# Kernel tuning notes

Hardware: AMD Instinct MI355X
Metric: run time of the kernel (lower is better)

## Reference

```python
import jax, jax.numpy as jnp
import numpy as np

N_WAY = 5
N_SHOT = 25
N_SUPPORT = N_WAY * N_SHOT  # 125
N_QUERY = 2048
D = 8192
C_REG = 0.1        # default C_reg of MetaOptNetHead_SVM_CS
MAX_ITER = 20      # default maxIter of QPFunction
SIGMA = 0.1        # centering parameter of the interior-point iteration


def setup_inputs() -> dict:
    key = jax.random.key(0)
    k1, k2, k3 = jax.random.split(key, 3)
    query = jax.random.normal(k1, (N_QUERY, D), dtype=jnp.float32)
    support = jax.random.normal(k2, (N_SUPPORT, D), dtype=jnp.float32)
    support_labels = jax.random.randint(k3, (N_SUPPORT,), 0, N_WAY, dtype=jnp.int32)
    scale = jnp.ones((1,), dtype=jnp.float32)  # nn.Parameter([1.0])
    return {
        "query": query,
        "support": support,
        "support_labels": support_labels,
        "n_way": N_WAY,
        "n_shot": N_SHOT,
        "scale": scale,
    }


def _solve_qp(G, e, h, A, b):
    """Solve min_z 0.5 z^T G z + e^T z  s.t.  z <= h (C = I),  A z = b.

    Primal-dual infeasible-start interior-point method with MAX_ITER fixed
    Newton steps (the jax analogue of qpth's QPFunction(maxIter=20)).
    Shapes: G (B,n,n), e (B,n), h (B,n), A (B,p,n), b (B,p).
    """
    B, n = e.shape
    p = b.shape[1]
    m = n  # C = I -> one inequality per variable
    At = jnp.swapaxes(A, 1, 2)                      # (B,n,p)
    zero_pp = jnp.zeros((B, p, p), dtype=G.dtype)
    A_row = jnp.concatenate([A, zero_pp], axis=2)   # (B,p,n+p), constant

    z = jnp.zeros_like(e)
    s = jnp.ones_like(h)
    lam = jnp.ones_like(h)
    nu = jnp.zeros_like(b)

    def frac_to_boundary(x, dx):
        # largest alpha in (0,1] keeping x + alpha*dx > 0
        ratio = jnp.where(dx < 0, -x / jnp.where(dx < 0, dx, -1.0), jnp.inf)
        return jnp.min(ratio, axis=1)

    def step(carry, _):
        z, s, lam, nu = carry
        Gz = jnp.einsum('bij,bj->bi', G, z)
        r1 = Gz + e + lam + jnp.einsum('bpi,bp->bi', A, nu)   # dual residual (C^T lam = lam)
        r2 = z + s - h                                         # primal ineq residual
        r4 = jnp.einsum('bpi,bi->bp', A, z) - b                # primal eq residual
        mu = SIGMA * jnp.sum(s * lam, axis=1, keepdims=True) / m
        r3 = lam * s - mu                                      # perturbed complementarity
        # Reduced KKT system: (G + diag(lam/s)) dz + A^T dnu = rhs1 ; A dz = -r4
        H = G + jax.vmap(jnp.diag)(lam / s)                    # (B,n,n)
        rhs1 = -(r1 + (lam * r2 - r3) / s)                     # (B,n)
        K = jnp.concatenate(
            [jnp.concatenate([H, At], axis=2), A_row], axis=1)  # (B,n+p,n+p)
        rhs = jnp.concatenate([rhs1, -r4], axis=1)             # (B,n+p)
        sol = jnp.linalg.solve(K, rhs[..., None])[..., 0]
        dz, dnu = sol[:, :n], sol[:, n:]
        ds = -r2 - dz
        dlam = (-r3 - lam * ds) / s
        alpha = jnp.minimum(
            1.0, 0.99 * jnp.minimum(frac_to_boundary(s, ds),
                                    frac_to_boundary(lam, dlam)))[:, None]
        return (z + alpha * dz, s + alpha * ds,
                lam + alpha * dlam, nu + alpha * dnu), None

    (z, s, lam, nu), _ = jax.lax.scan(step, (z, s, lam, nu), None, length=MAX_ITER)
    return z


def _svm_cs_head(query, support, support_labels, n_way):
    support_b = support[None]            # (1, ns, d) -- head unsqueezes batch dim
    query_b = query[None]                # (1, nq, d)
    B, ns, _ = support_b.shape
    f32 = jnp.float32

    # Gram matrix of support, then kron with I_{n_way} (batched_kronecker == jnp.kron)
    K = jnp.einsum('bnd,bmd->bnm', support_b, support_b)            # (B,ns,ns)
    eye_w = jnp.eye(n_way, dtype=f32)
    G = jax.vmap(lambda k: jnp.kron(k, eye_w))(K)                    # (B,ns*nw,ns*nw)
    G = G + jnp.eye(n_way * ns, dtype=f32)[None]

    y1h = jax.nn.one_hot(support_labels, n_way, dtype=f32).reshape(B, ns * n_way)
    e = -y1h
    h = C_REG * y1h
    A = jnp.kron(jnp.eye(ns, dtype=f32), jnp.ones((1, n_way), f32))[None]  # (1,ns,ns*nw)
    b = jnp.zeros((B, ns), f32)

    qp_sol = _solve_qp(G, e, h, A, b)                                # (B, ns*nw)

    compat = jnp.einsum('bnd,bqd->bnq', support_b, query_b)          # (B,ns,nq)
    qp3 = qp_sol.reshape(B, ns, n_way)
    # logits[b,q,w] = sum_s qp3[b,s,w] * compat[b,s,q]
    logits = jnp.einsum('bsw,bsq->bqw', qp3, compat)                 # (B,nq,nw)
    num_sv = jnp.sum(jnp.any(qp3 > 0.001, axis=2))                   # support-vector count
    return logits, num_sv


def reference(query, support, support_labels, n_way, n_shot, scale):
    logits, num_sv = _svm_cs_head(query, support, support_labels, n_way)
    return scale * logits, num_sv
```

## Files before the change

kernel.cpp:

```cpp
#include <hip/hip_runtime.h>

#define NS   125
#define NW   5
#define NQ   2048
#define DD   8192
#define CREG 0.1f
#define PGD_ITERS 16

#define OFF_PART 0
#define OFF_K    1000000
#define OFF_QP3  1016000
#define OFF_W    1017000

__global__ __launch_bounds__(256) void gram_partial(const float* __restrict__ support,
                                                    float* __restrict__ part) {
    __shared__ __align__(16) float As[128][68];
    __shared__ __align__(16) float Bs[128][68];
    const int tid = threadIdx.x;
    const int c  = blockIdx.x;
    const int qy = blockIdx.y, qz = blockIdx.z;
    const int d0 = c * 128;
    const int sy0 = qy * 64, sz0 = qz * 64;
    for (int idx = tid; idx < 64 * 128; idx += 256) {
        int sl = idx >> 7, dj = idx & 127;
        int sa = sy0 + sl, sb = sz0 + sl;
        As[dj][sl] = (sa < NS) ? support[(size_t)sa * DD + d0 + dj] : 0.f;
        Bs[dj][sl] = (sb < NS) ? support[(size_t)sb * DD + d0 + dj] : 0.f;
    }
    __syncthreads();
    const int tx = tid & 15, ty = tid >> 4;
    float acc[4][4];
#pragma unroll
    for (int i = 0; i < 4; i++)
#pragma unroll
        for (int j = 0; j < 4; j++) acc[i][j] = 0.f;
#pragma unroll 4
    for (int d = 0; d < 128; ++d) {
        float4 a = *(const float4*)&As[d][tx * 4];
        float4 b = *(const float4*)&Bs[d][ty * 4];
        float av[4] = {a.x, a.y, a.z, a.w};
        float bv[4] = {b.x, b.y, b.z, b.w};
#pragma unroll
        for (int i = 0; i < 4; i++)
#pragma unroll
            for (int j = 0; j < 4; j++) acc[i][j] += av[i] * bv[j];
    }
    float* dst = part + (size_t)c * (NS * NS);
#pragma unroll
    for (int i = 0; i < 4; i++) {
        int gi = sy0 + tx * 4 + i;
        if (gi >= NS) continue;
#pragma unroll
        for (int j = 0; j < 4; j++) {
            int gj = sz0 + ty * 4 + j;
            if (gj < NS) dst[gi * NS + gj] = acc[i][j];
        }
    }
}

__global__ __launch_bounds__(256) void gram_reduce(const float* __restrict__ part,
                                                   float* __restrict__ Kg) {
    int t = blockIdx.x * 256 + threadIdx.x;
    if (t < NS * NS) {
        float s = 0.f;
        for (int c = 0; c < 64; ++c) s += part[(size_t)c * (NS * NS) + t];
        Kg[t] = s;
    }
}

__global__ __launch_bounds__(256) void qp_solve(const float* __restrict__ Kg,
                                                const int* __restrict__ labels,
                                                float* __restrict__ qp3,
                                                float* __restrict__ outNumSv) {
    __shared__ __align__(16) float zs[NW][128];
    __shared__ float red2[128 * 25];
    __shared__ float rsmax[2];
    __shared__ int svcount;

    const int tid  = threadIdx.x;
    const int w    = tid >> 6;
    const int lane = tid & 63;
    const int c0   = w * 32;
    const int r0   = lane, r1 = lane + 64;

    float kr0[32], kr1[32];
#pragma unroll
    for (int j = 0; j < 32; ++j) {
        const int col = c0 + j;
        const bool cv = (col < NS);
        kr0[j] = cv ? Kg[col * NS + r0] : 0.f;
        kr1[j] = (cv && r1 < NS) ? Kg[col * NS + r1] : 0.f;
    }
    for (int idx = tid; idx < NW * 128; idx += 256) ((float*)zs)[idx] = 0.f;
    if (tid == 0) svcount = 0;
    float rsum0 = 0.f, rsum1 = 0.f;
#pragma unroll
    for (int j = 0; j < 32; ++j) { rsum0 += fabsf(kr0[j]); rsum1 += fabsf(kr1[j]); }
    red2[r0 * 25 + w * 5] = rsum0;
    red2[r1 * 25 + w * 5] = rsum1;
    __syncthreads();
    const int prow = w * 64 + lane;
    if (w < 2) {
        const float* rr = &red2[prow * 25];
        float t = (prow < NS) ? rr[0] + rr[5] + rr[10] + rr[15] : 0.f;
#pragma unroll
        for (int off = 32; off; off >>= 1) t = fmaxf(t, __shfl_xor(t, off));
        if (lane == 0) rsmax[w] = t;
    }
    __syncthreads();
    const float eta = 1.9f / (fmaxf(rsmax[0], rsmax[1]) + 1.0f);
    const int lab = (w < 2 && prow < NS) ? labels[prow] : 0;
    float z[NW] = {0.f, 0.f, 0.f, 0.f, 0.f};

    for (int it = 0; it < PGD_ITERS; ++it) {
        float acc0[NW] = {0.f, 0.f, 0.f, 0.f, 0.f};
        float acc1[NW] = {0.f, 0.f, 0.f, 0.f, 0.f};
#pragma unroll
        for (int c = 0; c < 8; ++c) {
            const int jb = c0 + 4 * c;
            float4 z0 = *(const float4*)&zs[0][jb];
            float4 z1 = *(const float4*)&zs[1][jb];
            float4 z2 = *(const float4*)&zs[2][jb];
            float4 z3 = *(const float4*)&zs[3][jb];
            float4 z4 = *(const float4*)&zs[4][jb];
            const float k00 = kr0[4*c], k01 = kr0[4*c+1], k02 = kr0[4*c+2], k03 = kr0[4*c+3];
            const float k10 = kr1[4*c], k11 = kr1[4*c+1], k12 = kr1[4*c+2], k13 = kr1[4*c+3];
            acc0[0] += k00*z0.x + k01*z0.y + k02*z0.z + k03*z0.w;
            acc0[1] += k00*z1.x + k01*z1.y + k02*z1.z + k03*z1.w;
            acc0[2] += k00*z2.x + k01*z2.y + k02*z2.z + k03*z2.w;
            acc0[3] += k00*z3.x + k01*z3.y + k02*z3.z + k03*z3.w;
            acc0[4] += k00*z4.x + k01*z4.y + k02*z4.z + k03*z4.w;
            acc1[0] += k10*z0.x + k11*z0.y + k12*z0.z + k13*z0.w;
            acc1[1] += k10*z1.x + k11*z1.y + k12*z1.z + k13*z1.w;
            acc1[2] += k10*z2.x + k11*z2.y + k12*z2.z + k13*z2.w;
            acc1[3] += k10*z3.x + k11*z3.y + k12*z3.z + k13*z3.w;
            acc1[4] += k10*z4.x + k11*z4.y + k12*z4.z + k13*z4.w;
        }
        {
            float* b0 = &red2[r0 * 25 + w * 5];
            b0[0] = acc0[0]; b0[1] = acc0[1]; b0[2] = acc0[2]; b0[3] = acc0[3]; b0[4] = acc0[4];
            float* b1 = &red2[r1 * 25 + w * 5];
            b1[0] = acc1[0]; b1[1] = acc1[1]; b1[2] = acc1[2]; b1[3] = acc1[3]; b1[4] = acc1[4];
        }
        __syncthreads();
        if (w < 2 && prow < NS) {
            const float* rr = &red2[prow * 25];
            float v[NW], h[NW];
#pragma unroll
            for (int a = 0; a < NW; a++) {
                float kz = rr[a] + rr[5 + a] + rr[10 + a] + rr[15 + a];
                float g = kz + z[a] - ((a == lab) ? 1.f : 0.f);
                v[a] = z[a] - eta * g;
                h[a] = (a == lab) ? CREG : 0.f;
            }
            float tau = fmaxf(fmaxf(fmaxf(v[0], v[1]), fmaxf(v[2], v[3])), v[4]);
#pragma unroll
            for (int n = 0; n < 7; ++n) {
                float g = 0.f, nf = 0.f;
#pragma unroll
                for (int a = 0; a < NW; a++) {
                    float d = v[a] - tau;
                    bool fr = (d <= h[a]);
                    g += fr ? d : h[a];
                    nf += fr ? 1.f : 0.f;
                }
                tau += g / nf;
            }
#pragma unroll
            for (int a = 0; a < NW; a++) {
                z[a] = fminf(v[a] - tau, h[a]);
                zs[a][prow] = z[a];
            }
        }
        __syncthreads();
    }

    if (w < 2 && prow < NS) {
        float m = fmaxf(fmaxf(fmaxf(z[0], z[1]), fmaxf(z[2], z[3])), z[4]);
        if (m > 0.001f) atomicAdd(&svcount, 1);
#pragma unroll
        for (int a = 0; a < NW; a++) qp3[prow * NW + a] = z[a];
    }
    __syncthreads();
    if (tid == 0) *outNumSv = (float)svcount;
}

__global__ __launch_bounds__(128) void w_kernel(const float* __restrict__ support,
                                                const float* __restrict__ qp3,
                                                float* __restrict__ W) {
    __shared__ float q3[NS * NW];
    const int tid = threadIdx.x;
    for (int i = tid; i < NS * NW; i += 128) q3[i] = qp3[i];
    __syncthreads();
    const int d = blockIdx.x * 128 + tid;
    float acc[NW] = {0.f, 0.f, 0.f, 0.f, 0.f};
    for (int sld = 0; sld < NS; ++sld) {
        float sv = support[(size_t)sld * DD + d];
#pragma unroll
        for (int a = 0; a < NW; a++) acc[a] += sv * q3[sld * NW + a];
    }
#pragma unroll
    for (int a = 0; a < NW; a++) W[(size_t)a * DD + d] = acc[a];
}

__global__ __launch_bounds__(256) void logits_kernel(const float* __restrict__ query,
                                                     const float* __restrict__ W,
                                                     const float* __restrict__ scale,
                                                     float* __restrict__ out) {
    const int tid = threadIdx.x;
    const int wave = tid >> 6, lane = tid & 63;
    const int q0 = blockIdx.x * 16 + wave * 4;
    float acc[4][NW];
#pragma unroll
    for (int j = 0; j < 4; j++)
#pragma unroll
        for (int a = 0; a < NW; a++) acc[j][a] = 0.f;
    const float4* qp[4];
#pragma unroll
    for (int j = 0; j < 4; j++) qp[j] = (const float4*)(query + (size_t)(q0 + j) * DD);
    for (int it = 0; it < 32; ++it) {
        int dv = it * 64 + lane;
        float4 qv[4];
#pragma unroll
        for (int j = 0; j < 4; j++) qv[j] = qp[j][dv];
#pragma unroll
        for (int a = 0; a < NW; a++) {
            float4 wv = ((const float4*)(W + (size_t)a * DD))[dv];
#pragma unroll
            for (int j = 0; j < 4; j++)
                acc[j][a] += qv[j].x * wv.x + qv[j].y * wv.y + qv[j].z * wv.z + qv[j].w * wv.w;
        }
    }
#pragma unroll
    for (int off = 32; off; off >>= 1) {
#pragma unroll
        for (int j = 0; j < 4; j++)
#pragma unroll
            for (int a = 0; a < NW; a++) acc[j][a] += __shfl_xor(acc[j][a], off);
    }
    if (lane == 0) {
        float sc = scale[0];
#pragma unroll
        for (int j = 0; j < 4; j++)
#pragma unroll
            for (int a = 0; a < NW; a++) out[(q0 + j) * NW + a] = sc * acc[j][a];
    }
}

extern "C" void kernel_launch(void* const* d_in, const int* in_sizes, int n_in,
                              void* d_out, int out_size, void* d_ws, size_t ws_size,
                              hipStream_t stream) {
    const float* query   = (const float*)d_in[0];
    const float* support = (const float*)d_in[1];
    const int*   labels  = (const int*)d_in[2];
    const float* scale   = (const float*)d_in[5];
    float* out = (float*)d_out;
    float* ws  = (float*)d_ws;

    float* part = ws + OFF_PART;
    float* Kg   = ws + OFF_K;
    float* qp3  = ws + OFF_QP3;
    float* W    = ws + OFF_W;

    hipLaunchKernelGGL(gram_partial, dim3(64, 2, 2), dim3(256), 0, stream, support, part);
    hipLaunchKernelGGL(gram_reduce, dim3(62), dim3(256), 0, stream, part, Kg);
    hipLaunchKernelGGL(qp_solve, dim3(1), dim3(256), 0, stream, Kg, labels, qp3, out + NQ * NW);
    hipLaunchKernelGGL(w_kernel, dim3(DD / 128), dim3(128), 0, stream, support, qp3, W);
    hipLaunchKernelGGL(logits_kernel, dim3(NQ / 16), dim3(256), 0, stream, query, W, scale, out);
}
```

Measured before the change: 195.0 us.

## Split logits GEMV over D into four chunks with separate reduction kernel

The logits kernel now splits the 8192-long dot products into four D-chunks, each block handling 8 queries (2 per wave) instead of 16, giving 1024 blocks instead of 128. Partial sums go to workspace and a small finish kernel adds the four partials and applies the scale. The aim is to spread the 64MB query read across more CUs to reach higher memory bandwidth, at the cost of an extra launch, a small partial-buffer round trip, and more repeated reads of W.

```diff
diff --git a/kernel.cpp b/kernel.cpp
--- a/kernel.cpp
+++ b/kernel.cpp
@@ -11,6 +11,7 @@
 #define OFF_K    1000000
 #define OFF_QP3  1016000
 #define OFF_W    1017000
+#define OFF_LP   1060000
 
 __global__ __launch_bounds__(256) void gram_partial(const float* __restrict__ support,
                                                     float* __restrict__ part) {
@@ -203,47 +204,54 @@
     for (int a = 0; a < NW; a++) W[(size_t)a * DD + d] = acc[a];
 }
 
-__global__ __launch_bounds__(256) void logits_kernel(const float* __restrict__ query,
-                                                     const float* __restrict__ W,
+__global__ __launch_bounds__(256) void logits_partial(const float* __restrict__ query,
+                                                      const float* __restrict__ W,
+                                                      float* __restrict__ lp) {
+    const int tid = threadIdx.x;
+    const int wave = tid >> 6, lane = tid & 63;
+    const int q0 = blockIdx.x * 8 + wave * 2;
+    const int q1 = q0 + 1;
+    const int chunk = blockIdx.y;
+    const int v0 = chunk * 512;
+    float a0[NW] = {0.f, 0.f, 0.f, 0.f, 0.f};
+    float a1[NW] = {0.f, 0.f, 0.f, 0.f, 0.f};
+    const float4* qp0 = (const float4*)(query + (size_t)q0 * DD);
+    const float4* qp1 = (const float4*)(query + (size_t)q1 * DD);
+    for (int it = 0; it < 8; ++it) {
+        int dv = v0 + it * 64 + lane;
+        float4 qv0 = qp0[dv];
+        float4 qv1 = qp1[dv];
+#pragma unroll
+        for (int a = 0; a < NW; a++) {
+            float4 wv = ((const float4*)(W + (size_t)a * DD))[dv];
+            a0[a] += qv0.x * wv.x + qv0.y * wv.y + qv0.z * wv.z + qv0.w * wv.w;
+            a1[a] += qv1.x * wv.x + qv1.y * wv.y + qv1.z * wv.z + qv1.w * wv.w;
+        }
+    }
+#pragma unroll
+    for (int off = 32; off; off >>= 1) {
+#pragma unroll
+        for (int a = 0; a < NW; a++) {
+            a0[a] += __shfl_xor(a0[a], off);
+            a1[a] += __shfl_xor(a1[a], off);
+        }
+    }
+    if (lane == 0) {
+        float* dst = lp + (size_t)chunk * (NQ * NW);
+#pragma unroll
+        for (int a = 0; a < NW; a++) dst[q0 * NW + a] = a0[a];
+#pragma unroll
+        for (int a = 0; a < NW; a++) dst[q1 * NW + a] = a1[a];
+    }
+}
+
+__global__ __launch_bounds__(256) void logits_finish(const float* __restrict__ lp,
                                                      const float* __restrict__ scale,
                                                      float* __restrict__ out) {
-    const int tid = threadIdx.x;
-    const int wave = tid >> 6, lane = tid & 63;
-    const int q0 = blockIdx.x * 16 + wave * 4;
-    float acc[4][NW];
-#pragma unroll
-    for (int j = 0; j < 4; j++)
-#pragma unroll
-        for (int a = 0; a < NW; a++) acc[j][a] = 0.f;
-    const float4* qp[4];
-#pragma unroll
-    for (int j = 0; j < 4; j++) qp[j] = (const float4*)(query + (size_t)(q0 + j) * DD);
-    for (int it = 0; it < 32; ++it) {
-        int dv = it * 64 + lane;
-        float4 qv[4];
-#pragma unroll
-        for (int j = 0; j < 4; j++) qv[j] = qp[j][dv];
-#pragma unroll
-        for (int a = 0; a < NW; a++) {
-            float4 wv = ((const float4*)(W + (size_t)a * DD))[dv];
-#pragma unroll
-            for (int j = 0; j < 4; j++)
-                acc[j][a] += qv[j].x * wv.x + qv[j].y * wv.y + qv[j].z * wv.z + qv[j].w * wv.w;
-        }
-    }
-#pragma unroll
-    for (int off = 32; off; off >>= 1) {
-#pragma unroll
-        for (int j = 0; j < 4; j++)
-#pragma unroll
-            for (int a = 0; a < NW; a++) acc[j][a] += __shfl_xor(acc[j][a], off);
-    }
-    if (lane == 0) {
-        float sc = scale[0];
-#pragma unroll
-        for (int j = 0; j < 4; j++)
-#pragma unroll
-            for (int a = 0; a < NW; a++) out[(q0 + j) * NW + a] = sc * acc[j][a];
+    int t = blockIdx.x * 256 + threadIdx.x;
+    if (t < NQ * NW) {
+        float s = lp[t] + lp[NQ * NW + t] + lp[2 * NQ * NW + t] + lp[3 * NQ * NW + t];
+        out[t] = scale[0] * s;
     }
 }
 
@@ -261,10 +269,12 @@
     float* Kg   = ws + OFF_K;
     float* qp3  = ws + OFF_QP3;
     float* W    = ws + OFF_W;
+    float* lp   = ws + OFF_LP;
 
     hipLaunchKernelGGL(gram_partial, dim3(64, 2, 2), dim3(256), 0, stream, support, part);
     hipLaunchKernelGGL(gram_reduce, dim3(62), dim3(256), 0, stream, part, Kg);
     hipLaunchKernelGGL(qp_solve, dim3(1), dim3(256), 0, stream, Kg, labels, qp3, out + NQ * NW);
     hipLaunchKernelGGL(w_kernel, dim3(DD / 128), dim3(128), 0, stream, support, qp3, W);
-    hipLaunchKernelGGL(logits_kernel, dim3(NQ / 16), dim3(256), 0, stream, query, W, scale, out);
-}
+    hipLaunchKernelGGL(logits_partial, dim3(NQ / 8, 4), dim3(256), 0, stream, query, W, lp);
+    hipLaunchKernelGGL(logits_finish, dim3((NQ * NW + 255) / 256), dim3(256), 0, stream, lp, scale, out);
+}
```

After: 175.7 us. 1.11x faster.
